# Kernel tuning notes

Hardware: AMD Instinct MI355X
Metric: run time of the kernel (lower is better)

## Reference

```python
import jax, jax.numpy as jnp
import numpy as np

B, S, D, H = 1, 256, 128, 4
HD = D // H          # 32
EPS = 1e-5
SCALE = 1.0 / float(np.sqrt(HD))


def setup_inputs() -> dict:
    key = jax.random.key(0)
    ks = jax.random.split(key, 6)
    pair = jax.random.normal(ks[0], (B, S, S, D), dtype=jnp.float32)
    ln_w = jnp.ones((D,), dtype=jnp.float32)
    wq = jax.random.normal(ks[1], (D, D), dtype=jnp.float32) * 0.05
    wk = jax.random.normal(ks[2], (D, D), dtype=jnp.float32) * 0.05
    wv = jax.random.normal(ks[3], (D, D), dtype=jnp.float32) * 0.05
    wo = jax.random.normal(ks[4], (D, D), dtype=jnp.float32) * 0.05
    return {"pair": pair, "ln_w": ln_w, "wq": wq, "wk": wk, "wv": wv, "wo": wo}


def reference(pair, ln_w, wq, wk, wv, wo):
    b, s, _, d = pair.shape
    h, hd = H, HD
    # LayerNorm (weight only, no bias) over last dim
    mu = jnp.mean(pair, axis=-1, keepdims=True)
    var = jnp.mean((pair - mu) ** 2, axis=-1, keepdims=True)
    xn = (pair - mu) * jax.lax.rsqrt(var + EPS) * ln_w
    # starting=True: no transpose of the pair axes
    q = (xn @ wq.T).reshape(b, s, s, h, hd)
    k = (xn @ wk.T).reshape(b, s, s, h, hd)
    v = (xn @ wv.T).reshape(b, s, s, h, hd)
    # attention over the second seq axis (j), independent per row i
    scores = jnp.einsum("biqhd,bikhd->bihqk", q, k) * SCALE  # [b,i,h,q,k]
    p = jax.nn.softmax(scores, axis=-1)
    out = jnp.einsum("bihqk,bikhd->biqhd", p, v).reshape(b, s, s, d)
    return out @ wo.T
```

## Files before the change

kernel.cpp:

```cpp
#include <hip/hip_runtime.h>
#include <hip/hip_bf16.h>
#include <math.h>

#define S 256
#define D 128
#define H 4
#define HD 32

constexpr float EPS = 1e-5f;
constexpr float EXPC = 0.17677669529663687f * 1.44269504088896f;

typedef short bf16x8 __attribute__((ext_vector_type(8)));
typedef float floatx4 __attribute__((ext_vector_type(4)));

union BfBits { __hip_bfloat16 b; unsigned short u; };
__device__ inline unsigned short f2bf_bits(float f) {
  BfBits t;
  t.b = __float2bfloat16(f);
  return t.u;
}
__device__ inline short f2bf_s(float f) { return (short)f2bf_bits(f); }
__device__ inline float bfbits2f(unsigned short u) {
  union { float f; unsigned int i; } t;
  t.i = ((unsigned int)u) << 16;
  return t.f;
}
__device__ inline void split_bf(float x, unsigned short& hi, unsigned short& lo) {
  hi = f2bf_bits(x);
  lo = f2bf_bits(x - bfbits2f(hi));
}
__device__ inline unsigned int pk2(float a, float b) {
  return (unsigned int)f2bf_bits(a) | ((unsigned int)f2bf_bits(b) << 16);
}

__global__ __launch_bounds__(256) void wsplit_kernel(
    const float* __restrict__ wq, const float* __restrict__ wk,
    const float* __restrict__ wv, const float* __restrict__ wo,
    unsigned short* __restrict__ whi, unsigned short* __restrict__ wlo) {
  int idx = blockIdx.x * 256 + threadIdx.x;
  const float* srcs[4] = {wq, wk, wv, wo};
#pragma unroll
  for (int m = 0; m < 4; m++) {
    unsigned short hi, lo;
    split_bf(srcs[m][idx], hi, lo);
    whi[m * 16384 + idx] = hi;
    wlo[m * 16384 + idx] = lo;
  }
}

#define XS(row, col) ((col) ^ (((row) & 7) << 3))

__device__ __forceinline__ floatx4 MF(bf16x8 a, bf16x8 b, floatx4 c) {
  return __builtin_amdgcn_mfma_f32_16x16x32_bf16(a, b, c, 0, 0, 0);
}

__device__ __forceinline__ void kv_produce(
    const unsigned short* xn, const unsigned short* __restrict__ Whi,
    const unsigned short* __restrict__ Wlo, unsigned short* base, int jt,
    int h, int hb, int c16, int quad) {
  unsigned short* Kt = base;
  unsigned short* Vt = base + 8192;
  const unsigned short* wkh = Whi + 16384;
  const unsigned short* wkl = Wlo + 16384;
  const unsigned short* wvh = Whi + 32768;
  const unsigned short* wvl = Wlo + 32768;
  const int arow = h * 32 + hb + c16;
  floatx4 ak[4], av[4];
#pragma unroll
  for (int nt = 0; nt < 4; nt++) {
    ak[nt] = (floatx4){0.f, 0.f, 0.f, 0.f};
    av[nt] = (floatx4){0.f, 0.f, 0.f, 0.f};
  }
#pragma unroll
  for (int ks = 0; ks < 4; ks++) {
    bf16x8 bh[4];
#pragma unroll
    for (int nt = 0; nt < 4; nt++) {
      const int row = jt * 64 + nt * 16 + c16;
      bh[nt] = *(const bf16x8*)&xn[row * D + XS(row, ks * 32 + quad * 8)];
    }
    bf16x8 kh = *(const bf16x8*)(wkh + arow * D + ks * 32 + quad * 8);
    bf16x8 kl = *(const bf16x8*)(wkl + arow * D + ks * 32 + quad * 8);
    bf16x8 vh = *(const bf16x8*)(wvh + arow * D + ks * 32 + quad * 8);
    bf16x8 vl = *(const bf16x8*)(wvl + arow * D + ks * 32 + quad * 8);
#pragma unroll
    for (int nt = 0; nt < 4; nt++) {
      ak[nt] = MF(kh, bh[nt], ak[nt]);
      ak[nt] = MF(kl, bh[nt], ak[nt]);
      av[nt] = MF(bh[nt], vh, av[nt]);
      av[nt] = MF(bh[nt], vl, av[nt]);
    }
  }
  const int c2 = (hb >> 3) + (quad >> 1);
#pragma unroll
  for (int nt = 0; nt < 4; nt++) {
    const int jl = nt * 16 + c16;
    ushort4 pkk;
    pkk.x = f2bf_bits(ak[nt][0]);
    pkk.y = f2bf_bits(ak[nt][1]);
    pkk.z = f2bf_bits(ak[nt][2]);
    pkk.w = f2bf_bits(ak[nt][3]);
    *(ushort4*)(Kt + h * 2048 + c2 * 512 + jl * 8 + (quad & 1) * 4) = pkk;
    ushort4 pv;
    pv.x = f2bf_bits(av[nt][0]);
    pv.y = f2bf_bits(av[nt][1]);
    pv.z = f2bf_bits(av[nt][2]);
    pv.w = f2bf_bits(av[nt][3]);
    *(ushort4*)(Vt + h * 2048 + (hb + c16) * 64 +
                (((nt * 2 + (quad >> 1)) ^ (c16 & 7)) << 3) + (quad & 1) * 4) =
        pv;
  }
}

__device__ __forceinline__ void attn_consume(const unsigned short* base, int h,
                                             int c16, int quad, int permc,
                                             const bf16x8 qf[8], floatx4 att0[8],
                                             floatx4 att1[8], float lsum[8]) {
  const unsigned short* Kt = base;
  const unsigned short* Vt = base + 8192;
#pragma unroll
  for (int jb = 0; jb < 2; jb++) {
    const int jbl = jb * 32;
    bf16x8 kf0 = *(const bf16x8*)(Kt + h * 2048 + quad * 512 + (jbl + permc) * 8);
    bf16x8 kf1 = *(const bf16x8*)(Kt + h * 2048 + quad * 512 + (jbl + permc + 4) * 8);
    const int ch = (jbl >> 3) + quad;
    bf16x8 vf0 = *(const bf16x8*)(Vt + h * 2048 + c16 * 64 + ((ch ^ (c16 & 7)) << 3));
    bf16x8 vf1 = *(const bf16x8*)(Vt + h * 2048 + (16 + c16) * 64 + ((ch ^ (c16 & 7)) << 3));
#pragma unroll
    for (int qt = 0; qt < 8; qt++) {
      floatx4 s0 = MF(kf0, qf[qt], (floatx4){0.f, 0.f, 0.f, 0.f});
      floatx4 s1 = MF(kf1, qf[qt], (floatx4){0.f, 0.f, 0.f, 0.f});
      float pr[8];
#pragma unroll
      for (int r = 0; r < 4; r++) pr[r] = exp2f(s0[r]);
#pragma unroll
      for (int r = 0; r < 4; r++) pr[4 + r] = exp2f(s1[r]);
      float ls = 0.f;
#pragma unroll
      for (int r = 0; r < 8; r++) ls += pr[r];
      lsum[qt] += ls;
      bf16x8 pf;
#pragma unroll
      for (int r = 0; r < 8; r++) pf[r] = f2bf_s(pr[r]);
      att0[qt] = MF(vf0, pf, att0[qt]);
      att1[qt] = MF(vf1, pf, att1[qt]);
    }
  }
}

__global__ __launch_bounds__(512, 2) void fused_tri_kernel(
    const float* __restrict__ pair, const float* __restrict__ ln_w,
    const unsigned short* __restrict__ Whi,
    const unsigned short* __restrict__ Wlo, float* __restrict__ out) {
  __shared__ unsigned int smem[32768];
  unsigned short* xn = (unsigned short*)smem;

  const int i = blockIdx.x;
  const int w = (int)(threadIdx.x >> 6);
  const int lane = (int)(threadIdx.x & 63);
  const int c16 = lane & 15;
  const int quad = lane >> 4;
  const int h = w >> 1;
  const int half = w & 1;
  const int hb = half * 16;

  {
    float4 w0 = *(const float4*)(ln_w + c16 * 8);
    float4 w1 = *(const float4*)(ln_w + c16 * 8 + 4);
    float4 xr0[8], xr1[8];
#pragma unroll
    for (int g = 0; g < 8; g++) {
      const int tok = w * 32 + g * 4 + quad;
      const float* src = pair + ((size_t)i * S + tok) * D + c16 * 8;
      xr0[g] = *(const float4*)(src);
      xr1[g] = *(const float4*)(src + 4);
    }
#pragma unroll
    for (int g = 0; g < 8; g++) {
      const int tok = w * 32 + g * 4 + quad;
      float4 x0 = xr0[g];
      float4 x1 = xr1[g];
      float s = (x0.x + x0.y) + (x0.z + x0.w) + (x1.x + x1.y) + (x1.z + x1.w);
      s += __shfl_xor(s, 1);
      s += __shfl_xor(s, 2);
      s += __shfl_xor(s, 4);
      s += __shfl_xor(s, 8);
      const float mu = s * (1.0f / D);
      float a[8];
      a[0] = x0.x - mu; a[1] = x0.y - mu; a[2] = x0.z - mu; a[3] = x0.w - mu;
      a[4] = x1.x - mu; a[5] = x1.y - mu; a[6] = x1.z - mu; a[7] = x1.w - mu;
      float vs = 0.f;
#pragma unroll
      for (int r = 0; r < 8; r++) vs = fmaf(a[r], a[r], vs);
      vs += __shfl_xor(vs, 1);
      vs += __shfl_xor(vs, 2);
      vs += __shfl_xor(vs, 4);
      vs += __shfl_xor(vs, 8);
      const float rinv = rsqrtf(vs * (1.0f / D) + EPS);
      const float wv8[8] = {w0.x, w0.y, w0.z, w0.w, w1.x, w1.y, w1.z, w1.w};
      unsigned int u[4];
#pragma unroll
      for (int r = 0; r < 4; r++) {
        unsigned int h0 = f2bf_bits(a[2 * r] * rinv * wv8[2 * r]);
        unsigned int h1 = f2bf_bits(a[2 * r + 1] * rinv * wv8[2 * r + 1]);
        u[r] = h0 | (h1 << 16);
      }
      uint4 st = {u[0], u[1], u[2], u[3]};
      *(uint4*)&xn[tok * D + XS(tok, c16 * 8)] = st;
    }
  }
  __syncthreads();

  bf16x8 qf[8];
  {
    bf16x8 qah[2][4], qal[2][4];
#pragma unroll
    for (int mi = 0; mi < 2; mi++)
#pragma unroll
      for (int ks = 0; ks < 4; ks++) {
        const int arow = h * 32 + mi * 16 + c16;
        qah[mi][ks] = *(const bf16x8*)(Whi + arow * D + ks * 32 + quad * 8);
        qal[mi][ks] = *(const bf16x8*)(Wlo + arow * D + ks * 32 + quad * 8);
      }
#pragma unroll
    for (int r = 0; r < 2; r++) {
      floatx4 acc[2][4];
#pragma unroll
      for (int mi = 0; mi < 2; mi++)
#pragma unroll
        for (int nt = 0; nt < 4; nt++) acc[mi][nt] = (floatx4){0.f, 0.f, 0.f, 0.f};
#pragma unroll
      for (int ks = 0; ks < 4; ks++) {
        bf16x8 bh[4];
#pragma unroll
        for (int nt = 0; nt < 4; nt++) {
          const int row = half * 128 + r * 64 + nt * 16 + c16;
          bh[nt] = *(const bf16x8*)&xn[row * D + XS(row, ks * 32 + quad * 8)];
        }
#pragma unroll
        for (int mi = 0; mi < 2; mi++)
#pragma unroll
          for (int nt = 0; nt < 4; nt++) {
            acc[mi][nt] = MF(qah[mi][ks], bh[nt], acc[mi][nt]);
            acc[mi][nt] = MF(qal[mi][ks], bh[nt], acc[mi][nt]);
          }
      }
      const int srcL = c16 + (quad & 1) * 32;
      const int srcH = srcL + 16;
      const bool hi2 = quad >= 2;
#pragma unroll
      for (int nt = 0; nt < 4; nt++) {
        int pa = (int)pk2(acc[0][nt][0] * EXPC, acc[0][nt][1] * EXPC);
        int pb = (int)pk2(acc[0][nt][2] * EXPC, acc[0][nt][3] * EXPC);
        int pc = (int)pk2(acc[1][nt][0] * EXPC, acc[1][nt][1] * EXPC);
        int pd = (int)pk2(acc[1][nt][2] * EXPC, acc[1][nt][3] * EXPC);
        int aL = __shfl(pa, srcL), cL = __shfl(pc, srcL);
        int bL = __shfl(pb, srcL), dL = __shfl(pd, srcL);
        int aH = __shfl(pa, srcH), cH = __shfl(pc, srcH);
        int bH = __shfl(pb, srcH), dH = __shfl(pd, srcH);
        union { unsigned int u[4]; bf16x8 v; } qq_;
        qq_.u[0] = (unsigned int)(hi2 ? cL : aL);
        qq_.u[1] = (unsigned int)(hi2 ? dL : bL);
        qq_.u[2] = (unsigned int)(hi2 ? cH : aH);
        qq_.u[3] = (unsigned int)(hi2 ? dH : bH);
        qf[r * 4 + nt] = qq_.v;
      }
    }
  }

  floatx4 att[2][8];
#pragma unroll
  for (int dt = 0; dt < 2; dt++)
#pragma unroll
    for (int qt = 0; qt < 8; qt++) att[dt][qt] = (floatx4){0.f, 0.f, 0.f, 0.f};
  float lsum[8] = {0.f, 0.f, 0.f, 0.f, 0.f, 0.f, 0.f, 0.f};
  const int permc = ((c16 >> 2) * 8) + (c16 & 3);

  unsigned short* kvb = (unsigned short*)(smem + 16384);
  kv_produce(xn, Whi, Wlo, kvb, 0, h, hb, c16, quad);
  __syncthreads();
  for (int jt = 0; jt < 4; jt++) {
    if (jt < 3)
      kv_produce(xn, Whi, Wlo, kvb + ((jt + 1) & 1) * 16384, jt + 1, h, hb,
                 c16, quad);
    attn_consume(kvb + (jt & 1) * 16384, h, c16, quad, permc, qf, att[0],
                 att[1], lsum);
    __syncthreads();
  }

#pragma unroll
  for (int qt = 0; qt < 8; qt++) {
    float l = lsum[qt];
    l += __shfl_xor(l, 16);
    l += __shfl_xor(l, 32);
    lsum[qt] = 1.0f / l;
  }

  unsigned short* Ohi = (unsigned short*)smem;
  unsigned short* Olo = (unsigned short*)smem + 32768;
#pragma unroll
  for (int t = 0; t < 8; t++) {
    const float inv = lsum[t];
    const int tokg = half * 128 + t * 16 + c16;
#pragma unroll
    for (int dt = 0; dt < 2; dt++) {
      floatx4 v4 = att[dt][t];
      const int gran = h * 4 + dt * 2 + (quad >> 1);
      const int addr = tokg * 128 + ((gran ^ (tokg & 7)) << 3) + (quad & 1) * 4;
      ushort4 h4, l4;
      split_bf(v4[0] * inv, h4.x, l4.x);
      split_bf(v4[1] * inv, h4.y, l4.y);
      split_bf(v4[2] * inv, h4.z, l4.z);
      split_bf(v4[3] * inv, h4.w, l4.w);
      *(ushort4*)&Ohi[addr] = h4;
      *(ushort4*)&Olo[addr] = l4;
    }
  }
  __syncthreads();

  const int g32 = w & 3;
  const int th = w >> 2;
  floatx4 oacc[2][8];
#pragma unroll
  for (int mi = 0; mi < 2; mi++)
#pragma unroll
    for (int nt = 0; nt < 8; nt++) oacc[mi][nt] = (floatx4){0.f, 0.f, 0.f, 0.f};
#pragma unroll
  for (int ks = 0; ks < 4; ks++) {
    bf16x8 wo_h[2], wo_l[2];
#pragma unroll
    for (int mi = 0; mi < 2; mi++) {
      const int m0 = g32 * 32 + mi * 16;
      wo_h[mi] = *(const bf16x8*)(Whi + 3 * 16384 + (m0 + c16) * D + ks * 32 + quad * 8);
      wo_l[mi] = *(const bf16x8*)(Wlo + 3 * 16384 + (m0 + c16) * D + ks * 32 + quad * 8);
    }
#pragma unroll
    for (int nt = 0; nt < 8; nt++) {
      const int tok = th * 128 + nt * 16 + c16;
      const int gran = ks * 4 + quad;
      const int addr = tok * 128 + ((gran ^ (tok & 7)) << 3);
      bf16x8 bh = *(const bf16x8*)&Ohi[addr];
      bf16x8 bl = *(const bf16x8*)&Olo[addr];
#pragma unroll
      for (int mi = 0; mi < 2; mi++) {
        oacc[mi][nt] = MF(wo_h[mi], bh, oacc[mi][nt]);
        oacc[mi][nt] = MF(wo_h[mi], bl, oacc[mi][nt]);
        oacc[mi][nt] = MF(wo_l[mi], bh, oacc[mi][nt]);
      }
    }
  }
#pragma unroll
  for (int nt = 0; nt < 8; nt++) {
    const int tok = th * 128 + nt * 16 + c16;
#pragma unroll
    for (int mi = 0; mi < 2; mi++) {
      float4 st4;
      st4.x = oacc[mi][nt][0];
      st4.y = oacc[mi][nt][1];
      st4.z = oacc[mi][nt][2];
      st4.w = oacc[mi][nt][3];
      *(float4*)(out + ((size_t)i * S + tok) * D + g32 * 32 + mi * 16 + quad * 4) = st4;
    }
  }
}

extern "C" void kernel_launch(void* const* d_in, const int* in_sizes, int n_in,
                              void* d_out, int out_size, void* d_ws,
                              size_t ws_size, hipStream_t stream) {
  const float* pair = (const float*)d_in[0];
  const float* ln_w = (const float*)d_in[1];
  const float* wq = (const float*)d_in[2];
  const float* wk = (const float*)d_in[3];
  const float* wv = (const float*)d_in[4];
  const float* wo = (const float*)d_in[5];
  float* out = (float*)d_out;

  unsigned short* Whi = (unsigned short*)d_ws;
  unsigned short* Wlo = Whi + 4 * 16384;

  wsplit_kernel<<<64, 256, 0, stream>>>(wq, wk, wv, wo, Whi, Wlo);
  fused_tri_kernel<<<S, 512, 0, stream>>>(pair, ln_w, Whi, Wlo, out);
}
```

Before: 135.6 us.

## Pre-permute Wq rows to drop Q-fragment shuffles; single-pass LayerNorm stats

The weight-split kernel now stores Wq with its output rows permuted so that the MFMA accumulator layout of the Q projection directly matches the operand layout needed for the score MFMA. This removes eight cross-lane shuffles and selects per Q fragment in the main kernel. LayerNorm now computes the sum and the sum of squares together, interleaving their reductions instead of running two dependent shuffle chains. The variance formula E[x^2]-mu^2 can lose precision through cancellation.

```diff
diff --git a/kernel.cpp b/kernel.cpp
--- a/kernel.cpp
+++ b/kernel.cpp
@@ -39,10 +39,13 @@
     unsigned short* __restrict__ whi, unsigned short* __restrict__ wlo) {
   int idx = blockIdx.x * 256 + threadIdx.x;
   const float* srcs[4] = {wq, wk, wv, wo};
+  const int d = idx >> 7, c = idx & 127;
+  const int hq = d >> 5, mi = (d >> 4) & 1, p = d & 15;
+  const int qsrc = (hq * 32 + ((p >> 2) << 3) + mi * 4 + (p & 3)) * 128 + c;
 #pragma unroll
   for (int m = 0; m < 4; m++) {
     unsigned short hi, lo;
-    split_bf(srcs[m][idx], hi, lo);
+    split_bf(srcs[m][m == 0 ? qsrc : idx], hi, lo);
     whi[m * 16384 + idx] = hi;
     wlo[m * 16384 + idx] = lo;
   }
@@ -181,22 +184,28 @@
       float4 x0 = xr0[g];
       float4 x1 = xr1[g];
       float s = (x0.x + x0.y) + (x0.z + x0.w) + (x1.x + x1.y) + (x1.z + x1.w);
+      float ss = x0.x * x0.x;
+      ss = fmaf(x0.y, x0.y, ss);
+      ss = fmaf(x0.z, x0.z, ss);
+      ss = fmaf(x0.w, x0.w, ss);
+      ss = fmaf(x1.x, x1.x, ss);
+      ss = fmaf(x1.y, x1.y, ss);
+      ss = fmaf(x1.z, x1.z, ss);
+      ss = fmaf(x1.w, x1.w, ss);
       s += __shfl_xor(s, 1);
+      ss += __shfl_xor(ss, 1);
       s += __shfl_xor(s, 2);
+      ss += __shfl_xor(ss, 2);
       s += __shfl_xor(s, 4);
+      ss += __shfl_xor(ss, 4);
       s += __shfl_xor(s, 8);
+      ss += __shfl_xor(ss, 8);
       const float mu = s * (1.0f / D);
+      const float var = fmaf(-mu, mu, ss * (1.0f / D));
+      const float rinv = rsqrtf(var + EPS);
       float a[8];
       a[0] = x0.x - mu; a[1] = x0.y - mu; a[2] = x0.z - mu; a[3] = x0.w - mu;
       a[4] = x1.x - mu; a[5] = x1.y - mu; a[6] = x1.z - mu; a[7] = x1.w - mu;
-      float vs = 0.f;
-#pragma unroll
-      for (int r = 0; r < 8; r++) vs = fmaf(a[r], a[r], vs);
-      vs += __shfl_xor(vs, 1);
-      vs += __shfl_xor(vs, 2);
-      vs += __shfl_xor(vs, 4);
-      vs += __shfl_xor(vs, 8);
-      const float rinv = rsqrtf(vs * (1.0f / D) + EPS);
       const float wv8[8] = {w0.x, w0.y, w0.z, w0.w, w1.x, w1.y, w1.z, w1.w};
       unsigned int u[4];
 #pragma unroll
@@ -245,24 +254,13 @@
             acc[mi][nt] = MF(qal[mi][ks], bh[nt], acc[mi][nt]);
           }
       }
-      const int srcL = c16 + (quad & 1) * 32;
-      const int srcH = srcL + 16;
-      const bool hi2 = quad >= 2;
 #pragma unroll
       for (int nt = 0; nt < 4; nt++) {
-        int pa = (int)pk2(acc[0][nt][0] * EXPC, acc[0][nt][1] * EXPC);
-        int pb = (int)pk2(acc[0][nt][2] * EXPC, acc[0][nt][3] * EXPC);
-        int pc = (int)pk2(acc[1][nt][0] * EXPC, acc[1][nt][1] * EXPC);
-        int pd = (int)pk2(acc[1][nt][2] * EXPC, acc[1][nt][3] * EXPC);
-        int aL = __shfl(pa, srcL), cL = __shfl(pc, srcL);
-        int bL = __shfl(pb, srcL), dL = __shfl(pd, srcL);
-        int aH = __shfl(pa, srcH), cH = __shfl(pc, srcH);
-        int bH = __shfl(pb, srcH), dH = __shfl(pd, srcH);
         union { unsigned int u[4]; bf16x8 v; } qq_;
-        qq_.u[0] = (unsigned int)(hi2 ? cL : aL);
-        qq_.u[1] = (unsigned int)(hi2 ? dL : bL);
-        qq_.u[2] = (unsigned int)(hi2 ? cH : aH);
-        qq_.u[3] = (unsigned int)(hi2 ? dH : bH);
+        qq_.u[0] = pk2(acc[0][nt][0] * EXPC, acc[0][nt][1] * EXPC);
+        qq_.u[1] = pk2(acc[0][nt][2] * EXPC, acc[0][nt][3] * EXPC);
+        qq_.u[2] = pk2(acc[1][nt][0] * EXPC, acc[1][nt][1] * EXPC);
+        qq_.u[3] = pk2(acc[1][nt][2] * EXPC, acc[1][nt][3] * EXPC);
         qf[r * 4 + nt] = qq_.v;
       }
     }
```

Result: no change. 136.7 us (+0.8%).
